# Kernel tuning notes

Hardware: AMD Instinct MI355X
Metric: run time of the kernel (lower is better)

The kernel has to match this reference:

```python
import jax, jax.numpy as jnp
import numpy as np

B, S, E, H = 4, 2048, 1024, 16
D = E // H  # head_size = 64


def setup_inputs() -> dict:
    key = jax.random.key(0)
    ks = jax.random.split(key, 5)
    x = jax.random.normal(ks[0], (B, S, E), dtype=jnp.float32)
    # nn.Linear default init ~ U(-1/sqrt(fan_in), 1/sqrt(fan_in))
    bound = 1.0 / np.sqrt(E)
    W_qkv = jax.random.uniform(ks[1], (E, 3 * E), dtype=jnp.float32, minval=-bound, maxval=bound)
    b_qkv = jax.random.uniform(ks[2], (3 * E,), dtype=jnp.float32, minval=-bound, maxval=bound)
    W_out = jax.random.uniform(ks[3], (E, E), dtype=jnp.float32, minval=-bound, maxval=bound)
    b_out = jax.random.uniform(ks[4], (E,), dtype=jnp.float32, minval=-bound, maxval=bound)
    return {"x": x, "W_qkv": W_qkv, "b_qkv": b_qkv, "W_out": W_out, "b_out": b_out, "mask": 1}


def reference(x, W_qkv, b_qkv, W_out, b_out, mask):
    qkv = x @ W_qkv + b_qkv                              # [B,S,3E]
    qkv = qkv.reshape(B, S, H, 3 * D).transpose(0, 2, 1, 3)  # [B,H,S,3D]
    q, k, v = jnp.split(qkv, 3, axis=-1)                  # each [B,H,S,D]
    scale = 1.0 / np.sqrt(E)  # NOTE: original divides by sqrt(n_embd), not sqrt(head_size)
    y = jnp.einsum('bhqd,bhkd->bhqk', q, k) * scale       # [B,H,S,S]
    if mask:
        causal = jnp.tril(jnp.ones((S, S), dtype=bool))
        y = jnp.where(causal, y, -1e9)
    y = jax.nn.softmax(y, axis=-1)
    vals = jnp.einsum('bhqk,bhkd->bhqd', y, v)            # [B,H,S,D]
    vals = vals.transpose(0, 2, 1, 3).reshape(B, S, E)
    return vals @ W_out + b_out
```

## Files before the change

### kernel.cpp

```cpp
#include <hip/hip_runtime.h>
#include <hip/hip_bf16.h>
#include <cstdint>
#include <cstddef>

typedef __bf16 bf16;
typedef __bf16 bf16x8 __attribute__((ext_vector_type(8)));
typedef float f32x4 __attribute__((ext_vector_type(4)));
typedef unsigned int u32x4 __attribute__((ext_vector_type(4)));
typedef unsigned int u32x2 __attribute__((ext_vector_type(2)));

#define DEVINL __device__ __forceinline__

namespace {
constexpr int Bb = 4, Ss = 2048, Ee = 1024, Hh = 16;
constexpr int Mm = Bb * Ss;
constexpr int N_QKV = 3 * Ee;
constexpr float SCQ = 0.03125f * 1.44269504f;
}

DEVINL void gl_lds16(const bf16* g, bf16* l) {
  __builtin_amdgcn_global_load_lds((const __attribute__((address_space(1))) void*)g,
                                   (__attribute__((address_space(3))) void*)l, 16, 0, 0);
}

DEVINL unsigned int pkbf(float a, float b) {
  bf16 x = (bf16)a, y = (bf16)b;
  return (unsigned int)__builtin_bit_cast(unsigned short, x) |
         ((unsigned int)__builtin_bit_cast(unsigned short, y) << 16);
}


__global__ void k_cvt_bf16(const float* __restrict__ in, bf16* __restrict__ out, int n) {
  int i = (blockIdx.x * 256 + threadIdx.x) * 8;
  if (i >= n) return;
  float4 a = *(const float4*)(in + i);
  float4 c = *(const float4*)(in + i + 4);
  bf16x8 v = {(bf16)a.x, (bf16)a.y, (bf16)a.z, (bf16)a.w,
              (bf16)c.x, (bf16)c.y, (bf16)c.z, (bf16)c.w};
  *(bf16x8*)(out + i) = v;
}

__global__ void k_transpose_cvt(const float* __restrict__ in, bf16* __restrict__ out, int R, int C) {
  __shared__ float tile[32][33];
  const int c0 = blockIdx.x * 32, r0 = blockIdx.y * 32;
  const int tx = threadIdx.x, ty = threadIdx.y;
  for (int i = 0; i < 32; i += 8)
    tile[ty + i][tx] = in[(size_t)(r0 + ty + i) * C + (c0 + tx)];
  __syncthreads();
  for (int i = 0; i < 32; i += 8)
    out[(size_t)(c0 + ty + i) * R + (r0 + tx)] = (bf16)tile[tx][ty + i];
}


__global__ __launch_bounds__(256) void k_qkv_gemm(const bf16* __restrict__ A,
                                                  const bf16* __restrict__ Bt,
                                                  const float* __restrict__ bias,
                                                  bf16* __restrict__ qbuf,
                                                  bf16* __restrict__ kbuf,
                                                  bf16* __restrict__ vtb) {
  __shared__ bf16 sm[2 * 128 * 64];
  bf16* As = sm;
  bf16* Bs = sm + 128 * 64;
  const int tid = threadIdx.x, wid = tid >> 6, lane = tid & 63;
  const int wm = wid >> 1, wn = wid & 1;
  const int fr = lane & 15, kg = lane >> 4;
  const int m0 = blockIdx.y * 128, n0 = blockIdx.x * 128;
  const int K = Ee;

  f32x4 acc[4][4] = {};

  const int ar = wid * 32 + (lane >> 3);
  const int ac = (lane & 7) * 8;
  const bf16* Ag = A + (size_t)(m0 + ar) * K + ac;
  const bf16* Bg = Bt + (size_t)(n0 + ar) * K + ac;
  bf16* AsW = As + wid * 32 * 64;
  bf16* BsW = Bs + wid * 32 * 64;

  for (int kt = 0; kt < K; kt += 64) {
    __syncthreads();
    for (int i = 0; i < 4; ++i) {
      gl_lds16(Ag + (size_t)(i * 8) * K + kt, AsW + i * 8 * 64);
      gl_lds16(Bg + (size_t)(i * 8) * K + kt, BsW + i * 8 * 64);
    }
    __syncthreads();
    for (int kk = 0; kk < 2; ++kk) {
      bf16x8 af[4], bfr[4];
      for (int mi = 0; mi < 4; ++mi)
        af[mi] = *(const bf16x8*)(As + (wm * 64 + mi * 16 + fr) * 64 + kk * 32 + kg * 8);
      for (int ni = 0; ni < 4; ++ni)
        bfr[ni] = *(const bf16x8*)(Bs + (wn * 64 + ni * 16 + fr) * 64 + kk * 32 + kg * 8);
      for (int mi = 0; mi < 4; ++mi)
        for (int ni = 0; ni < 4; ++ni)
          acc[mi][ni] = __builtin_amdgcn_mfma_f32_16x16x32_bf16(af[mi], bfr[ni], acc[mi][ni], 0, 0, 0);
    }
  }
  const int row_b = m0 >> 11;
  const int s_base = (m0 & 2047) + wm * 64;
  for (int ni = 0; ni < 4; ++ni) {
    const int col0 = n0 + wn * 64 + ni * 16;
    const int h = col0 / 192;
    const int w192 = col0 - h * 192;
    const int cls = w192 >> 6;
    const float bv = bias[col0 + fr];
    if (cls == 2) {
      const int d = w192 - 128 + fr;
      bf16* dst = vtb + (((size_t)row_b * Hh + h) * 64 + d) * Ss + s_base;
      for (int mi = 0; mi < 4; ++mi) {
        u32x2 pk2 = {pkbf(acc[mi][ni][0] + bv, acc[mi][ni][1] + bv),
                     pkbf(acc[mi][ni][2] + bv, acc[mi][ni][3] + bv)};
        *(u32x2*)(dst + mi * 16 + kg * 4) = pk2;
      }
    } else {
      bf16* buf = (cls == 0) ? qbuf : kbuf;
      const float sc = (cls == 0) ? SCQ : 1.f;
      const int d = (w192 & 63) + fr;
      bf16* dst = buf + (((size_t)row_b * Hh + h) * Ss + s_base) * 64 + d;
      for (int mi = 0; mi < 4; ++mi)
        for (int r = 0; r < 4; ++r)
          dst[(size_t)(mi * 16 + kg * 4 + r) * 64] = (bf16)((acc[mi][ni][r] + bv) * sc);
    }
  }
}

__global__ __launch_bounds__(256) void k_out_gemm(const bf16* __restrict__ A,
                                                  const bf16* __restrict__ Bt,
                                                  const float* __restrict__ bias,
                                                  float* __restrict__ out) {
  __shared__ bf16 sm[2 * 128 * 64];
  bf16* As = sm;
  bf16* Bs = sm + 128 * 64;
  const int tid = threadIdx.x, wid = tid >> 6, lane = tid & 63;
  const int wm = wid >> 1, wn = wid & 1;
  const int fr = lane & 15, kg = lane >> 4;
  const int m0 = blockIdx.y * 128, n0 = blockIdx.x * 128;
  const int K = Ee;

  f32x4 acc[4][4] = {};

  const int ar = wid * 32 + (lane >> 3);
  const int ac = (lane & 7) * 8;
  const bf16* Ag = A + (size_t)(m0 + ar) * K + ac;
  const bf16* Bg = Bt + (size_t)(n0 + ar) * K + ac;
  bf16* AsW = As + wid * 32 * 64;
  bf16* BsW = Bs + wid * 32 * 64;

  for (int kt = 0; kt < K; kt += 64) {
    __syncthreads();
    for (int i = 0; i < 4; ++i) {
      gl_lds16(Ag + (size_t)(i * 8) * K + kt, AsW + i * 8 * 64);
      gl_lds16(Bg + (size_t)(i * 8) * K + kt, BsW + i * 8 * 64);
    }
    __syncthreads();
    for (int kk = 0; kk < 2; ++kk) {
      bf16x8 af[4], bfr[4];
      for (int mi = 0; mi < 4; ++mi)
        af[mi] = *(const bf16x8*)(As + (wm * 64 + mi * 16 + fr) * 64 + kk * 32 + kg * 8);
      for (int ni = 0; ni < 4; ++ni)
        bfr[ni] = *(const bf16x8*)(Bs + (wn * 64 + ni * 16 + fr) * 64 + kk * 32 + kg * 8);
      for (int mi = 0; mi < 4; ++mi)
        for (int ni = 0; ni < 4; ++ni)
          acc[mi][ni] = __builtin_amdgcn_mfma_f32_16x16x32_bf16(af[mi], bfr[ni], acc[mi][ni], 0, 0, 0);
    }
  }
  for (int ni = 0; ni < 4; ++ni) {
    const int col = n0 + wn * 64 + ni * 16 + fr;
    const float bv = bias[col];
    for (int mi = 0; mi < 4; ++mi) {
      const int mbase = m0 + wm * 64 + mi * 16 + kg * 4;
      for (int r = 0; r < 4; ++r)
        out[(size_t)(mbase + r) * Ee + col] = acc[mi][ni][r] + bv;
    }
  }
}


__global__ __launch_bounds__(256, 3) void k_attn(const bf16* __restrict__ qbuf,
                                                 const bf16* __restrict__ kbuf,
                                                 const bf16* __restrict__ vtb,
                                                 bf16* __restrict__ vals) {
  const int g = blockIdx.x;
  const int qt = 15 - (g >> 6);
  const int bh = g & 63;
  const int b = bh >> 4, h = bh & 15;
  const int q0 = qt * 128;
  const int tid = threadIdx.x, w = tid >> 6, lane = tid & 63;
  const int fr = lane & 15, kg = lane >> 4;
  const int rl = lane >> 3, cl = (lane & 7) ^ (lane >> 3);

  __shared__ bf16 KsB[2][4096];
  __shared__ bf16 VtB[2][4096];

  const bf16* qb = qbuf + (size_t)bh * Ss * 64;
  const bf16* kb = kbuf + (size_t)bh * Ss * 64 + (size_t)rl * 64 + cl * 8;
  const bf16* vb = vtb + (size_t)bh * 64 * Ss + (size_t)rl * Ss + cl * 8;

  const int gA = (kg & 1) * 32 + fr;
  const int gB = gA + 16;
  const bool hiSel = (kg >> 1) != 0;

  bf16x8 aq[2][2];
  for (int sub = 0; sub < 2; ++sub) {
    const bf16* qr = qb + (size_t)(q0 + w * 32 + sub * 16 + fr) * 64 + kg * 8;
    aq[sub][0] = *(const bf16x8*)(qr);
    aq[sub][1] = *(const bf16x8*)(qr + 32);
  }

  float m_run[2] = {-1e30f, -1e30f}, l_run[2] = {0.f, 0.f};
  f32x4 o_acc[2][4] = {};

  const int nt = 2 * qt + 2;

  for (int t = 0; t < 2; ++t) {
    const int i = w * 2 + t;
    gl_lds16(kb + (size_t)(i * 8) * 64, KsB[0] + i * 512);
    gl_lds16(vb + (size_t)(i * 8) * Ss, VtB[0] + i * 512);
  }

  int cur = 0;
  for (int it = 0; it < nt; ++it) {
    const int kv0 = it * 64;
    __syncthreads();
    if (it + 1 < nt) {
      const int kvn = kv0 + 64;
      for (int t = 0; t < 2; ++t) {
        const int i = w * 2 + t;
        gl_lds16(kb + (size_t)(kvn + i * 8) * 64, KsB[cur ^ 1] + i * 512);
        gl_lds16(vb + (size_t)(i * 8) * Ss + kvn, VtB[cur ^ 1] + i * 512);
      }
    }
    const bool active = (kv0 <= q0 + w * 32 + 31);
    if (active) {
      f32x4 sacc[2][4] = {};
      for (int kk = 0; kk < 2; ++kk) {
        bf16x8 bk[4];
        for (int ni = 0; ni < 4; ++ni) {
          const int rb = ni * 16 + fr;
          bk[ni] = *(const bf16x8*)(KsB[cur] + rb * 64 + (((kk * 4 + kg) ^ (rb & 7)) * 8));
        }
        __builtin_amdgcn_s_setprio(1);
        for (int sub = 0; sub < 2; ++sub)
          for (int ni = 0; ni < 4; ++ni)
            sacc[sub][ni] =
                __builtin_amdgcn_mfma_f32_16x16x32_bf16(bk[ni], aq[sub][kk], sacc[sub][ni], 0, 0, 0);
        __builtin_amdgcn_s_setprio(0);
      }
      bf16x8 bp[2][2];
      for (int sub = 0; sub < 2; ++sub) {
        const int qs = q0 + w * 32 + sub * 16;
        float p[4][4];
        float mnew = -1e30f;
        if (kv0 + 63 > qs) {
          const int q = qs + fr;
          for (int ni = 0; ni < 4; ++ni)
            for (int r = 0; r < 4; ++r) {
              const int k = kv0 + ni * 16 + kg * 4 + r;
              float s = sacc[sub][ni][r];
              if (k > q) s = -1e30f;
              p[ni][r] = s;
              mnew = fmaxf(mnew, s);
            }
        } else {
          for (int ni = 0; ni < 4; ++ni)
            for (int r = 0; r < 4; ++r) {
              float s = sacc[sub][ni][r];
              p[ni][r] = s;
              mnew = fmaxf(mnew, s);
            }
        }
        mnew = fmaxf(mnew, __shfl_xor(mnew, 16, 64));
        mnew = fmaxf(mnew, __shfl_xor(mnew, 32, 64));
        float mn;
        if (__all(mnew - m_run[sub] <= 8.f)) {
          mn = m_run[sub];
        } else {
          mn = fmaxf(m_run[sub], mnew);
          const float fs = exp2f(m_run[sub] - mn);
          m_run[sub] = mn;
          l_run[sub] *= fs;
          for (int ni = 0; ni < 4; ++ni)
            for (int r = 0; r < 4; ++r)
              o_acc[sub][ni][r] *= fs;
        }
        float rs = 0.f;
        for (int ni = 0; ni < 4; ++ni)
          for (int r = 0; r < 4; ++r) {
            const float e = exp2f(p[ni][r] - mn);
            p[ni][r] = e;
            rs += e;
          }
        rs += __shfl_xor(rs, 16, 64);
        rs += __shfl_xor(rs, 32, 64);
        l_run[sub] += rs;
        unsigned int Wlo[4], Whi[4];
        for (int ni = 0; ni < 4; ++ni) {
          Wlo[ni] = pkbf(p[ni][0], p[ni][1]);
          Whi[ni] = pkbf(p[ni][2], p[ni][3]);
        }
        for (int kk = 0; kk < 2; ++kk) {
          const int i0 = 2 * kk, i1 = 2 * kk + 1;
          unsigned int a0 = (unsigned int)__shfl((int)Wlo[i0], gA, 64);
          unsigned int a1 = (unsigned int)__shfl((int)Wlo[i1], gA, 64);
          unsigned int b0 = (unsigned int)__shfl((int)Whi[i0], gA, 64);
          unsigned int b1 = (unsigned int)__shfl((int)Whi[i1], gA, 64);
          unsigned int c0 = (unsigned int)__shfl((int)Wlo[i0], gB, 64);
          unsigned int c1 = (unsigned int)__shfl((int)Wlo[i1], gB, 64);
          unsigned int d0 = (unsigned int)__shfl((int)Whi[i0], gB, 64);
          unsigned int d1 = (unsigned int)__shfl((int)Whi[i1], gB, 64);
          u32x4 wv = {hiSel ? a1 : a0, hiSel ? b1 : b0, hiSel ? c1 : c0, hiSel ? d1 : d0};
          bp[sub][kk] = __builtin_bit_cast(bf16x8, wv);
        }
      }
      for (int kk = 0; kk < 2; ++kk) {
        bf16x8 bv[4];
        for (int ni = 0; ni < 4; ++ni) {
          const int rb = ni * 16 + fr;
          bv[ni] = *(const bf16x8*)(VtB[cur] + rb * 64 + (((kk * 4 + kg) ^ (rb & 7)) * 8));
        }
        __builtin_amdgcn_s_setprio(1);
        for (int sub = 0; sub < 2; ++sub)
          for (int ni = 0; ni < 4; ++ni)
            o_acc[sub][ni] =
                __builtin_amdgcn_mfma_f32_16x16x32_bf16(bv[ni], bp[sub][kk], o_acc[sub][ni], 0, 0, 0);
        __builtin_amdgcn_s_setprio(0);
      }
    }
    cur ^= 1;
  }

  for (int sub = 0; sub < 2; ++sub) {
    const float inv = 1.f / l_run[sub];
    const int q = q0 + w * 32 + sub * 16 + fr;
    bf16* dst = vals + ((size_t)b * Ss + q) * Ee + h * 64 + kg * 4;
    for (int ni = 0; ni < 4; ++ni) {
      u32x2 pk2 = {pkbf(o_acc[sub][ni][0] * inv, o_acc[sub][ni][1] * inv),
                   pkbf(o_acc[sub][ni][2] * inv, o_acc[sub][ni][3] * inv)};
      *(u32x2*)(dst + ni * 16) = pk2;
    }
  }
}


extern "C" void kernel_launch(void* const* d_in, const int* in_sizes, int n_in,
                              void* d_out, int out_size, void* d_ws, size_t ws_size,
                              hipStream_t stream) {
  const float* x    = (const float*)d_in[0];
  const float* Wqkv = (const float*)d_in[1];
  const float* bqkv = (const float*)d_in[2];
  const float* Wout = (const float*)d_in[3];
  const float* bout = (const float*)d_in[4];
  float* out = (float*)d_out;

  char* ws = (char*)d_ws;
  const size_t MiB = 1048576, KiB = 1024;
  bf16* x_bf  = (bf16*)(ws);
  bf16* valsb = (bf16*)(ws);
  bf16* WqkvT = (bf16*)(ws + 16 * MiB);
  bf16* WoutT = (bf16*)(ws + 22 * MiB);
  bf16* qbuf  = (bf16*)(ws + 24 * MiB);
  bf16* kbuf  = (bf16*)(ws + 40 * MiB + 192 * KiB);
  bf16* vtb   = (bf16*)(ws + 56 * MiB + 384 * KiB);

  k_cvt_bf16<<<dim3(Mm * Ee / 2048), dim3(256), 0, stream>>>(x, x_bf, Mm * Ee);
  k_transpose_cvt<<<dim3(N_QKV / 32, Ee / 32), dim3(32, 8), 0, stream>>>(Wqkv, WqkvT, Ee, N_QKV);
  k_transpose_cvt<<<dim3(Ee / 32, Ee / 32), dim3(32, 8), 0, stream>>>(Wout, WoutT, Ee, Ee);
  k_qkv_gemm<<<dim3(N_QKV / 128, Mm / 128), dim3(256), 0, stream>>>(x_bf, WqkvT, bqkv, qbuf, kbuf, vtb);
  k_attn<<<dim3(Ss / 128 * Hh * Bb), dim3(256), 0, stream>>>(qbuf, kbuf, vtb, valsb);
  k_out_gemm<<<dim3(Ee / 128, Mm / 128), dim3(256), 0, stream>>>(valsb, WoutT, bout, out);
}
```

Before: 208.0 us.

## Restructure projection GEMMs with double-buffered LDS, swizzle, and larger 512-thread tiles

Replaces both projection GEMMs with a shared templated core that uses 256-row tiles and 512 threads (8 waves). The K loop double-buffers LDS with async global-to-LDS loads issued two tiles ahead, and uses explicit vmcnt waits and barriers instead of full syncthreads. An XOR swizzle on LDS columns targets bank conflicts, and s_setprio raises wave priority during the MFMA phase. The goal is to hide global load latency and raise operand reuse per block, at the cost of more registers and LDS per block and hand-tuned waitcnt values that must match the number of issued loads.

```diff
diff --git a/kernel.cpp b/kernel.cpp
--- a/kernel.cpp
+++ b/kernel.cpp
@@ -52,123 +52,135 @@
 }
 
 
-__global__ __launch_bounds__(256) void k_qkv_gemm(const bf16* __restrict__ A,
-                                                  const bf16* __restrict__ Bt,
-                                                  const float* __restrict__ bias,
-                                                  bf16* __restrict__ qbuf,
-                                                  bf16* __restrict__ kbuf,
-                                                  bf16* __restrict__ vtb) {
-  __shared__ bf16 sm[2 * 128 * 64];
-  bf16* As = sm;
-  bf16* Bs = sm + 128 * 64;
-  const int tid = threadIdx.x, wid = tid >> 6, lane = tid & 63;
-  const int wm = wid >> 1, wn = wid & 1;
+template <int NF>
+DEVINL void gemm_core256(const bf16* __restrict__ A, const bf16* __restrict__ Bt,
+                         int m0, int n0, bf16* As, bf16* Bs, f32x4 (&acc)[8][NF]) {
+  constexpr int K = 1024;
+  constexpr int TILEA = 16384;
+  constexpr int TILEB = NF * 4096;
+  const int tid = threadIdx.x;
+  const int w = tid >> 6, lane = tid & 63;
+  const int wm = w >> 2, wn = w & 3;
   const int fr = lane & 15, kg = lane >> 4;
-  const int m0 = blockIdx.y * 128, n0 = blockIdx.x * 128;
-  const int K = Ee;
-
-  f32x4 acc[4][4] = {};
-
-  const int ar = wid * 32 + (lane >> 3);
-  const int ac = (lane & 7) * 8;
-  const bf16* Ag = A + (size_t)(m0 + ar) * K + ac;
-  const bf16* Bg = Bt + (size_t)(n0 + ar) * K + ac;
-  bf16* AsW = As + wid * 32 * 64;
-  bf16* BsW = Bs + wid * 32 * 64;
-
-  for (int kt = 0; kt < K; kt += 64) {
-    __syncthreads();
-    for (int i = 0; i < 4; ++i) {
-      gl_lds16(Ag + (size_t)(i * 8) * K + kt, AsW + i * 8 * 64);
-      gl_lds16(Bg + (size_t)(i * 8) * K + kt, BsW + i * 8 * 64);
-    }
-    __syncthreads();
+  const int gc = (tid & 7) ^ ((tid >> 3) & 7);
+  const int srow = tid >> 3;
+  const bf16* Ag = A + (size_t)(m0 + srow) * K + gc * 8;
+  const bf16* Bg = Bt + (size_t)(n0 + srow) * K + gc * 8;
+  bf16* AdW = As + w * 512;
+  bf16* BdW = Bs + w * 512;
+
+#define STAGE_TILE(kt, buf)                                                       \
+  {                                                                               \
+    for (int i = 0; i < 4; ++i)                                                   \
+      gl_lds16(Ag + (kt) + (size_t)(i * 64) * K, AdW + (buf) * TILEA + i * 4096); \
+    for (int i = 0; i < NF; ++i)                                                  \
+      gl_lds16(Bg + (kt) + (size_t)(i * 64) * K, BdW + (buf) * TILEB + i * 4096); \
+  }
+
+  STAGE_TILE(0, 0)
+  STAGE_TILE(64, 1)
+  constexpr int nt = K / 64;
+  for (int t = 0; t < nt; ++t) {
+    const int cur = t & 1;
+    if constexpr (NF == 3) {
+      asm volatile("s_waitcnt vmcnt(7)" ::: "memory");
+    } else {
+      asm volatile("s_waitcnt vmcnt(6)" ::: "memory");
+    }
+    __builtin_amdgcn_sched_barrier(0);
+    __builtin_amdgcn_s_barrier();
+    __builtin_amdgcn_sched_barrier(0);
+    bf16x8 af[2][8], bfx[2][NF];
+    const bf16* Ab = As + cur * TILEA;
+    const bf16* Bb = Bs + cur * TILEB;
     for (int kk = 0; kk < 2; ++kk) {
-      bf16x8 af[4], bfr[4];
-      for (int mi = 0; mi < 4; ++mi)
-        af[mi] = *(const bf16x8*)(As + (wm * 64 + mi * 16 + fr) * 64 + kk * 32 + kg * 8);
-      for (int ni = 0; ni < 4; ++ni)
-        bfr[ni] = *(const bf16x8*)(Bs + (wn * 64 + ni * 16 + fr) * 64 + kk * 32 + kg * 8);
-      for (int mi = 0; mi < 4; ++mi)
-        for (int ni = 0; ni < 4; ++ni)
-          acc[mi][ni] = __builtin_amdgcn_mfma_f32_16x16x32_bf16(af[mi], bfr[ni], acc[mi][ni], 0, 0, 0);
-    }
-  }
+      const int sw = ((kk * 4 + kg) ^ (fr & 7)) * 8;
+      for (int mi = 0; mi < 8; ++mi)
+        af[kk][mi] = *(const bf16x8*)(Ab + (wm * 128 + mi * 16 + fr) * 64 + sw);
+      for (int ni = 0; ni < NF; ++ni)
+        bfx[kk][ni] = *(const bf16x8*)(Bb + (wn * (NF * 16) + ni * 16 + fr) * 64 + sw);
+    }
+    asm volatile("s_waitcnt lgkmcnt(0)" ::: "memory");
+    __builtin_amdgcn_sched_barrier(0);
+    __builtin_amdgcn_s_barrier();
+    __builtin_amdgcn_sched_barrier(0);
+    if (t + 2 < nt) STAGE_TILE((t + 2) * 64, cur)
+    __builtin_amdgcn_s_setprio(1);
+    for (int kk = 0; kk < 2; ++kk)
+      for (int mi = 0; mi < 8; ++mi)
+        for (int ni = 0; ni < NF; ++ni)
+          acc[mi][ni] =
+              __builtin_amdgcn_mfma_f32_16x16x32_bf16(af[kk][mi], bfx[kk][ni], acc[mi][ni], 0, 0, 0);
+    __builtin_amdgcn_s_setprio(0);
+  }
+#undef STAGE_TILE
+}
+
+__global__ __launch_bounds__(512, 2) void k_qkv_gemm(const bf16* __restrict__ A,
+                                                     const bf16* __restrict__ Bt,
+                                                     const float* __restrict__ bias,
+                                                     bf16* __restrict__ qbuf,
+                                                     bf16* __restrict__ kbuf,
+                                                     bf16* __restrict__ vtb) {
+  __shared__ bf16 As[2 * 16384];
+  __shared__ bf16 Bs[2 * 3 * 4096];
+  const int m0 = blockIdx.y * 256, n0 = blockIdx.x * 192;
+  f32x4 acc[8][3] = {};
+  gemm_core256<3>(A, Bt, m0, n0, As, Bs, acc);
+
+  const int tid = threadIdx.x, w = tid >> 6, lane = tid & 63;
+  const int wm = w >> 2, wn = w & 3;
+  const int fr = lane & 15, kg = lane >> 4;
   const int row_b = m0 >> 11;
-  const int s_base = (m0 & 2047) + wm * 64;
-  for (int ni = 0; ni < 4; ++ni) {
-    const int col0 = n0 + wn * 64 + ni * 16;
+  for (int ni = 0; ni < 3; ++ni) {
+    const int col0 = n0 + wn * 48 + ni * 16;
     const int h = col0 / 192;
     const int w192 = col0 - h * 192;
     const int cls = w192 >> 6;
     const float bv = bias[col0 + fr];
     if (cls == 2) {
       const int d = w192 - 128 + fr;
-      bf16* dst = vtb + (((size_t)row_b * Hh + h) * 64 + d) * Ss + s_base;
-      for (int mi = 0; mi < 4; ++mi) {
+      bf16* dstb = vtb + (((size_t)row_b * Hh + h) * 64 + d) * Ss;
+      for (int mi = 0; mi < 8; ++mi) {
+        const int s0 = (m0 & 2047) + wm * 128 + mi * 16 + kg * 4;
         u32x2 pk2 = {pkbf(acc[mi][ni][0] + bv, acc[mi][ni][1] + bv),
                      pkbf(acc[mi][ni][2] + bv, acc[mi][ni][3] + bv)};
-        *(u32x2*)(dst + mi * 16 + kg * 4) = pk2;
+        *(u32x2*)(dstb + s0) = pk2;
       }
     } else {
       bf16* buf = (cls == 0) ? qbuf : kbuf;
       const float sc = (cls == 0) ? SCQ : 1.f;
       const int d = (w192 & 63) + fr;
-      bf16* dst = buf + (((size_t)row_b * Hh + h) * Ss + s_base) * 64 + d;
-      for (int mi = 0; mi < 4; ++mi)
+      bf16* dstb = buf + ((size_t)row_b * Hh + h) * Ss * 64 + d;
+      for (int mi = 0; mi < 8; ++mi) {
+        const int s0 = (m0 & 2047) + wm * 128 + mi * 16 + kg * 4;
         for (int r = 0; r < 4; ++r)
-          dst[(size_t)(mi * 16 + kg * 4 + r) * 64] = (bf16)((acc[mi][ni][r] + bv) * sc);
-    }
-  }
-}
-
-__global__ __launch_bounds__(256) void k_out_gemm(const bf16* __restrict__ A,
-                                                  const bf16* __restrict__ Bt,
-                                                  const float* __restrict__ bias,
-                                                  float* __restrict__ out) {
-  __shared__ bf16 sm[2 * 128 * 64];
-  bf16* As = sm;
-  bf16* Bs = sm + 128 * 64;
-  const int tid = threadIdx.x, wid = tid >> 6, lane = tid & 63;
-  const int wm = wid >> 1, wn = wid & 1;
+          dstb[(size_t)(s0 + r) * 64] = (bf16)((acc[mi][ni][r] + bv) * sc);
+      }
+    }
+  }
+}
+
+__global__ __launch_bounds__(512, 2) void k_out_gemm(const bf16* __restrict__ A,
+                                                     const bf16* __restrict__ Bt,
+                                                     const float* __restrict__ bias,
+                                                     float* __restrict__ out) {
+  __shared__ bf16 As[2 * 16384];
+  __shared__ bf16 Bs[2 * 2 * 4096];
+  const int m0 = blockIdx.y * 256, n0 = blockIdx.x * 128;
+  f32x4 acc[8][2] = {};
+  gemm_core256<2>(A, Bt, m0, n0, As, Bs, acc);
+
+  const int tid = threadIdx.x, w = tid >> 6, lane = tid & 63;
+  const int wm = w >> 2, wn = w & 3;
   const int fr = lane & 15, kg = lane >> 4;
-  const int m0 = blockIdx.y * 128, n0 = blockIdx.x * 128;
-  const int K = Ee;
-
-  f32x4 acc[4][4] = {};
-
-  const int ar = wid * 32 + (lane >> 3);
-  const int ac = (lane & 7) * 8;
-  const bf16* Ag = A + (size_t)(m0 + ar) * K + ac;
-  const bf16* Bg = Bt + (size_t)(n0 + ar) * K + ac;
-  bf16* AsW = As + wid * 32 * 64;
-  bf16* BsW = Bs + wid * 32 * 64;
-
-  for (int kt = 0; kt < K; kt += 64) {
-    __syncthreads();
-    for (int i = 0; i < 4; ++i) {
-      gl_lds16(Ag + (size_t)(i * 8) * K + kt, AsW + i * 8 * 64);
-      gl_lds16(Bg + (size_t)(i * 8) * K + kt, BsW + i * 8 * 64);
-    }
-    __syncthreads();
-    for (int kk = 0; kk < 2; ++kk) {
-      bf16x8 af[4], bfr[4];
-      for (int mi = 0; mi < 4; ++mi)
-        af[mi] = *(const bf16x8*)(As + (wm * 64 + mi * 16 + fr) * 64 + kk * 32 + kg * 8);
-      for (int ni = 0; ni < 4; ++ni)
-        bfr[ni] = *(const bf16x8*)(Bs + (wn * 64 + ni * 16 + fr) * 64 + kk * 32 + kg * 8);
-      for (int mi = 0; mi < 4; ++mi)
-        for (int ni = 0; ni < 4; ++ni)
-          acc[mi][ni] = __builtin_amdgcn_mfma_f32_16x16x32_bf16(af[mi], bfr[ni], acc[mi][ni], 0, 0, 0);
-    }
-  }
-  for (int ni = 0; ni < 4; ++ni) {
-    const int col = n0 + wn * 64 + ni * 16 + fr;
+  for (int ni = 0; ni < 2; ++ni) {
+    const int col = n0 + wn * 32 + ni * 16 + fr;
     const float bv = bias[col];
-    for (int mi = 0; mi < 4; ++mi) {
-      const int mbase = m0 + wm * 64 + mi * 16 + kg * 4;
+    for (int mi = 0; mi < 8; ++mi) {
+      const int mb = m0 + wm * 128 + mi * 16 + kg * 4;
       for (int r = 0; r < 4; ++r)
-        out[(size_t)(mbase + r) * Ee + col] = acc[mi][ni][r] + bv;
+        out[(size_t)(mb + r) * Ee + col] = acc[mi][ni][r] + bv;
     }
   }
 }
@@ -363,7 +375,7 @@
   k_cvt_bf16<<<dim3(Mm * Ee / 2048), dim3(256), 0, stream>>>(x, x_bf, Mm * Ee);
   k_transpose_cvt<<<dim3(N_QKV / 32, Ee / 32), dim3(32, 8), 0, stream>>>(Wqkv, WqkvT, Ee, N_QKV);
   k_transpose_cvt<<<dim3(Ee / 32, Ee / 32), dim3(32, 8), 0, stream>>>(Wout, WoutT, Ee, Ee);
-  k_qkv_gemm<<<dim3(N_QKV / 128, Mm / 128), dim3(256), 0, stream>>>(x_bf, WqkvT, bqkv, qbuf, kbuf, vtb);
+  k_qkv_gemm<<<dim3(N_QKV / 192, Mm / 256), dim3(512), 0, stream>>>(x_bf, WqkvT, bqkv, qbuf, kbuf, vtb);
   k_attn<<<dim3(Ss / 128 * Hh * Bb), dim3(256), 0, stream>>>(qbuf, kbuf, vtb, valsb);
-  k_out_gemm<<<dim3(Ee / 128, Mm / 128), dim3(256), 0, stream>>>(valsb, WoutT, bout, out);
-}
+  k_out_gemm<<<dim3(Ee / 128, Mm / 256), dim3(512), 0, stream>>>(valsb, WoutT, bout, out);
+}
```

After: 191.3 us. 8.0% less time.
